# Optimization experiments

Measured on AMD Instinct MI355X. Metric: run time of the kernel, lower is better.

Reference implementation:

```python
import jax, jax.numpy as jnp
import numpy as np

B, D, H, S = 4096, 512, 512, 16
EVENT_THRESH = 0.85  # hard-coded in original forward (e_t > 0.85), tau unused


def setup_inputs() -> dict:
    key = jax.random.key(0)
    ks = jax.random.split(key, 17)
    s = 0.02
    return {
        "x_t": jax.random.normal(ks[0], (B, D), jnp.float32),
        "h_lstm": jax.random.normal(ks[1], (B, H), jnp.float32),
        "c_lstm": jax.random.normal(ks[2], (B, H), jnp.float32),
        "slots": jax.random.normal(ks[3], (B, S, D), jnp.float32),
        "ptr": jax.random.randint(ks[4], (B,), 0, S, jnp.int32),
        # SequenceMemoryCell params
        "value_W": jax.random.normal(ks[5], (D, D), jnp.float32) * s,
        "value_b": jnp.zeros((D,), jnp.float32),
        "ed_W": jax.random.normal(ks[6], (1, D), jnp.float32) * s,
        "ed_b": jnp.zeros((1,), jnp.float32),
        "pos_emb": jax.random.normal(ks[7], (S, D), jnp.float32),
        "lstm_Wih": jax.random.normal(ks[8], (4 * H, D), jnp.float32) * s,
        "lstm_Whh": jax.random.normal(ks[9], (4 * H, H), jnp.float32) * s,
        "lstm_bih": jnp.zeros((4 * H,), jnp.float32),
        "lstm_bhh": jnp.zeros((4 * H,), jnp.float32),
        # outer hand-written LSTM params
        "Wih": jax.random.normal(ks[10], (4 * H, D + H), jnp.float32) * s,
        "bih": jnp.zeros((4 * H,), jnp.float32),
        "Whh": jax.random.normal(ks[11], (4 * H, H), jnp.float32) * s,
    }


def reference(x_t, h_lstm, c_lstm, slots, value_W, value_b, ed_W, ed_b,
              pos_emb, lstm_Wih, lstm_Whh, lstm_bih, lstm_bhh,
              Wih, bih, Whh, ptr):
    b, n_slots, d = slots.shape
    h = lstm_Whh.shape[1]
    # --- SequenceMemoryCell ---
    e_t = jax.nn.sigmoid(x_t @ ed_W.T + ed_b)            # (B, 1)
    event = e_t > EVENT_THRESH                            # (B, 1) bool
    v = x_t @ value_W.T + value_b                         # (B, D)
    # conditional pointer-indexed write into circular slot buffer
    write = (jnp.arange(n_slots)[None, :] == ptr[:, None]) & event  # (B, S)
    new_slots = jnp.where(write[:, :, None], v[:, None, :], slots)
    new_ptr = (ptr + event[:, 0].astype(ptr.dtype)) % n_slots
    slots_pe = new_slots + pos_emb[None, :, :]            # (B, S, D)
    # slot-fuser LSTM over n_slots (PyTorch gate order i,f,g,o), h0=c0=0
    def step(carry, x_s):
        hh, cc = carry
        g = x_s @ lstm_Wih.T + lstm_bih + hh @ lstm_Whh.T + lstm_bhh
        i, f, gg, o = jnp.split(g, 4, axis=1)
        cc = jax.nn.sigmoid(f) * cc + jax.nn.sigmoid(i) * jnp.tanh(gg)
        hh = jax.nn.sigmoid(o) * jnp.tanh(cc)
        return (hh, cc), None
    h0 = jnp.zeros((b, h), slots.dtype)
    (h_mem, _), _ = jax.lax.scan(step, (h0, h0), jnp.swapaxes(slots_pe, 0, 1))
    # --- outer hand-written LSTM cell on [x_t; h_mem] ---
    gates = jnp.concatenate([x_t, h_mem], axis=1) @ Wih.T + bih + h_lstm @ Whh.T
    i, f, g_t, o = jnp.split(gates, 4, axis=1)
    c_new = jax.nn.sigmoid(f) * c_lstm + jax.nn.sigmoid(i) * jnp.tanh(g_t)
    h_new = jax.nn.sigmoid(o) * jnp.tanh(c_new)
    return (h_new, c_new, h_mem, new_slots, new_ptr)
```

## Files before the change

### kernel.cpp

```cpp
#include <hip/hip_runtime.h>
#include <hip/hip_bf16.h>

constexpr int kB = 4096;
constexpr int kD = 512;
constexpr int kH = 512;
constexpr int kS = 16;
constexpr int kG = 2048;

typedef __attribute__((ext_vector_type(8))) short bf16x8_t;
typedef __attribute__((ext_vector_type(4))) float f32x4_t;

__device__ __forceinline__ short f2bf(float x) {
  __hip_bfloat16 h = __float2bfloat16(x);
  return *reinterpret_cast<short*>(&h);
}
__device__ __forceinline__ float sigm(float x) { return 1.0f / (1.0f + expf(-x)); }

__global__ void event_kernel(const float* __restrict__ x,
                             const float* __restrict__ edW,
                             const float* __restrict__ edb,
                             const int* __restrict__ ptr,
                             int* __restrict__ ev,
                             float* __restrict__ newptr_out)
{
  int b = blockIdx.x * 4 + (threadIdx.x >> 6);
  int lane = threadIdx.x & 63;
  const float* xr = x + (size_t)b * kD;
  float sum = 0.f;
  for (int k = lane; k < kD; k += 64) sum += xr[k] * edW[k];
  #pragma unroll
  for (int off = 32; off; off >>= 1) sum += __shfl_down(sum, off, 64);
  if (lane == 0) {
    float e = sigm(sum + edb[0]);
    int evt = (e > 0.85f) ? 1 : 0;
    ev[b] = evt;
    newptr_out[b] = (float)((ptr[b] + evt) & (kS - 1));
  }
}

__global__ void f2b_kernel(const float* __restrict__ src, short* __restrict__ dst, int n4)
{
  int i = blockIdx.x * blockDim.x + threadIdx.x;
  if (i >= n4) return;
  const float4 v = reinterpret_cast<const float4*>(src)[i];
  short4 o;
  o.x = f2bf(v.x); o.y = f2bf(v.y); o.z = f2bf(v.z); o.w = f2bf(v.w);
  reinterpret_cast<short4*>(dst)[i] = o;
}

__global__ void packw_gates_kernel(const float* __restrict__ W1, int w1,
                                   const float* __restrict__ W2, int w2,
                                   short* __restrict__ dst, int total4)
{
  int i = blockIdx.x * blockDim.x + threadIdx.x;
  if (i >= total4) return;
  long e = (long)i * 4;
  int K = w1 + w2;
  long p = e / K;
  int col = (int)(e - p * K);
  long r = (long)(((p >> 4) & 3) * 512 + ((p >> 6) << 4) + (p & 15));
  const float* src = (col < w1) ? (W1 + r * (long)w1 + col)
                                : (W2 + r * (long)w2 + (col - w1));
  const float4 v = *reinterpret_cast<const float4*>(src);
  short4 o; o.x=f2bf(v.x); o.y=f2bf(v.y); o.z=f2bf(v.z); o.w=f2bf(v.w);
  *reinterpret_cast<short4*>(dst + e) = o;
}

__global__ void packbias_kernel(const float* __restrict__ b1, const float* __restrict__ b2,
                                float* __restrict__ o, int n)
{
  int p = blockIdx.x * blockDim.x + threadIdx.x;
  if (p >= n) return;
  int r = ((p >> 4) & 3) * 512 + ((p >> 6) << 4) + (p & 15);
  float v = b1[r];
  if (b2) v += b2[r];
  o[p] = v;
}

__global__ void slot_update_kernel(const float* __restrict__ slots,
                                   const float* __restrict__ v,
                                   const float* __restrict__ pos_emb,
                                   const int* __restrict__ ptr,
                                   const int* __restrict__ ev,
                                   float* __restrict__ new_slots,
                                   short* __restrict__ slots_pe)
{
  size_t i = (size_t)blockIdx.x * blockDim.x + threadIdx.x;
  size_t e = i * 4;
  int d = (int)(e & (kD - 1));
  size_t bs = e >> 9;
  int s = (int)(bs & (kS - 1));
  size_t b = bs >> 4;
  float4 val;
  if (ev[b] && (ptr[b] == s)) val = *reinterpret_cast<const float4*>(v + (b << 9) + d);
  else                        val = *reinterpret_cast<const float4*>(slots + e);
  *reinterpret_cast<float4*>(new_slots + e) = val;
  const float4 pe = *reinterpret_cast<const float4*>(pos_emb + ((size_t)s << 9) + d);
  short4 o;
  o.x = f2bf(val.x + pe.x); o.y = f2bf(val.y + pe.y);
  o.z = f2bf(val.z + pe.z); o.w = f2bf(val.w + pe.w);
  *reinterpret_cast<short4*>(slots_pe + e) = o;
}

__global__ __launch_bounds__(256)
void gemm_fused_kernel(const short* __restrict__ A0, int lda0,
                       const short* __restrict__ A1, int lda1,
                       const short* __restrict__ A2, int lda2,
                       int nseg, const short* __restrict__ W, int ldw,
                       const float* __restrict__ bias, int mode,
                       float* __restrict__ C, int ldc,
                       float* __restrict__ cbuf, short* __restrict__ hb,
                       float* __restrict__ hmem, int first, int last,
                       const float* __restrict__ c_in,
                       float* __restrict__ h_out, float* __restrict__ c_out)
{
  __shared__ short As[128 * 64];
  __shared__ short Ws[128 * 64];
  const int tid  = threadIdx.x;
  const int wave = tid >> 6;
  const int lane = tid & 63;
  const int wr = wave >> 1;
  const int wc = wave & 1;
  const int row0 = blockIdx.x * 128;
  const int col0 = blockIdx.y * 128;
  const int K = nseg << 9;

  f32x4_t acc[4][4];
  #pragma unroll
  for (int m = 0; m < 4; ++m)
    #pragma unroll
    for (int n = 0; n < 4; ++n)
      acc[m][n] = {0.f, 0.f, 0.f, 0.f};

  const int sr = lane >> 3;
  const int sc = (lane & 7) * 8;

  for (int k0 = 0; k0 < K; k0 += 64) {
    const int seg = k0 >> 9;
    const int ks  = k0 & 511;
    const short* Ap = (seg == 0) ? A0 : ((seg == 1) ? A1 : A2);
    const int   lda = (seg == 0) ? lda0 : ((seg == 1) ? lda1 : lda2);
    __syncthreads();
    #pragma unroll
    for (int j = 0; j < 4; ++j) {
      const int arow = wave * 32 + j * 8 + sr;
      const short* asrc = Ap + (size_t)(row0 + arow) * lda + ks + sc;
      __builtin_amdgcn_global_load_lds(
          (const __attribute__((address_space(1))) void*)asrc,
          (__attribute__((address_space(3))) void*)&As[(wave * 32 + j * 8) * 64],
          16, 0, 0);
      const short* wsrc = W + (size_t)(col0 + arow) * ldw + k0 + sc;
      __builtin_amdgcn_global_load_lds(
          (const __attribute__((address_space(1))) void*)wsrc,
          (__attribute__((address_space(3))) void*)&Ws[(wave * 32 + j * 8) * 64],
          16, 0, 0);
    }
    __syncthreads();
    #pragma unroll
    for (int kk = 0; kk < 64; kk += 32) {
      bf16x8_t af[4], bfr[4];
      const int kcol = kk + (lane >> 4) * 8;
      const int ar = wr * 64 + (lane & 15);
      const int br = wc * 64 + (lane & 15);
      #pragma unroll
      for (int m = 0; m < 4; ++m)
        af[m] = *reinterpret_cast<const bf16x8_t*>(&As[(ar + m * 16) * 64 + kcol]);
      #pragma unroll
      for (int n = 0; n < 4; ++n)
        bfr[n] = *reinterpret_cast<const bf16x8_t*>(&Ws[(br + n * 16) * 64 + kcol]);
      #pragma unroll
      for (int m = 0; m < 4; ++m)
        #pragma unroll
        for (int n = 0; n < 4; ++n)
          acc[m][n] = __builtin_amdgcn_mfma_f32_16x16x32_bf16(af[m], bfr[n], acc[m][n], 0, 0, 0);
    }
  }

  float bv[4];
  #pragma unroll
  for (int n = 0; n < 4; ++n)
    bv[n] = bias[col0 + wc * 64 + n * 16 + (lane & 15)];

  if (mode == 0) {
    #pragma unroll
    for (int n = 0; n < 4; ++n) {
      const int col = col0 + wc * 64 + n * 16 + (lane & 15);
      #pragma unroll
      for (int m = 0; m < 4; ++m) {
        const int rbase = row0 + wr * 64 + m * 16 + (lane >> 4) * 4;
        #pragma unroll
        for (int r = 0; r < 4; ++r)
          C[(size_t)(rbase + r) * ldc + col] = acc[m][n][r] + bv[n];
      }
    }
    return;
  }

  const int hcol = ((col0 >> 6) + wc) * 16 + (lane & 15);
  #pragma unroll
  for (int m = 0; m < 4; ++m) {
    const int rbase = row0 + wr * 64 + m * 16 + (lane >> 4) * 4;
    #pragma unroll
    for (int r = 0; r < 4; ++r) {
      const size_t idx = (size_t)(rbase + r) * kH + hcol;
      const float gi = acc[m][0][r] + bv[0];
      const float gf = acc[m][1][r] + bv[1];
      const float gg = acc[m][2][r] + bv[2];
      const float go = acc[m][3][r] + bv[3];
      float cp;
      if (mode == 1) cp = first ? 0.f : cbuf[idx];
      else           cp = c_in[idx];
      const float cn = sigm(gf) * cp + sigm(gi) * tanhf(gg);
      const float hn = sigm(go) * tanhf(cn);
      if (mode == 1) {
        cbuf[idx] = cn;
        hb[idx] = f2bf(hn);
        if (last) hmem[idx] = hn;
      } else {
        c_out[idx] = cn;
        h_out[idx] = hn;
      }
    }
  }
}

extern "C" void kernel_launch(void* const* d_in, const int* in_sizes, int n_in,
                              void* d_out, int out_size, void* d_ws, size_t ws_size,
                              hipStream_t stream)
{
  const float* x_t      = (const float*)d_in[0];
  const float* h_lstm   = (const float*)d_in[1];
  const float* c_lstm   = (const float*)d_in[2];
  const float* slots    = (const float*)d_in[3];
  const int*   ptr      = (const int*)  d_in[4];
  const float* value_W  = (const float*)d_in[5];
  const float* value_b  = (const float*)d_in[6];
  const float* ed_W     = (const float*)d_in[7];
  const float* ed_b     = (const float*)d_in[8];
  const float* pos_emb  = (const float*)d_in[9];
  const float* lstm_Wih = (const float*)d_in[10];
  const float* lstm_Whh = (const float*)d_in[11];
  const float* lstm_bih = (const float*)d_in[12];
  const float* lstm_bhh = (const float*)d_in[13];
  const float* Wih      = (const float*)d_in[14];
  const float* bih      = (const float*)d_in[15];
  const float* Whh      = (const float*)d_in[16];

  float* out       = (float*)d_out;
  float* h_new     = out;
  float* c_new     = out + (size_t)kB * kH;
  float* h_mem     = out + (size_t)2 * kB * kH;
  float* new_slots = out + (size_t)3 * kB * kH;
  float* new_ptr   = out + (size_t)3 * kB * kH + (size_t)kB * kS * kD;

  char* ws = (char*)d_ws;
  size_t off = 0;
  auto alloc = [&](size_t bytes) { void* p = ws + off; off += (bytes + 255) & ~(size_t)255; return p; };
  int*   ev        = (int*)  alloc((size_t)kB * 4);
  short* x_b       = (short*)alloc((size_t)kB * kD * 2);
  short* hlstm_b   = (short*)alloc((size_t)kB * kH * 2);
  short* vW_b      = (short*)alloc((size_t)kD * kD * 2);
  short* stepW_b   = (short*)alloc((size_t)kG * (kD + kH) * 2);
  float* stepBias  = (float*)alloc((size_t)kG * 4);
  short* outerW_b  = (short*)alloc((size_t)kG * (kD + kH + kH) * 2);
  float* outerBias = (float*)alloc((size_t)kG * 4);
  float* v_f32     = (float*)alloc((size_t)kB * kD * 4);
  short* h_b       = (short*)alloc((size_t)kB * kH * 2);
  float* c_f32     = (float*)alloc((size_t)kB * kH * 4);
  short* slots_pe  = (short*)alloc((size_t)kB * kS * kD * 2);
  (void)ws_size; (void)in_sizes; (void)n_in; (void)out_size;

  event_kernel<<<kB / 4, 256, 0, stream>>>(x_t, ed_W, ed_b, ptr, ev, new_ptr);

  f2b_kernel<<<(kB * kD / 4 + 255) / 256, 256, 0, stream>>>(x_t, x_b, kB * kD / 4);
  f2b_kernel<<<(kB * kH / 4 + 255) / 256, 256, 0, stream>>>(h_lstm, hlstm_b, kB * kH / 4);
  f2b_kernel<<<(kD * kD / 4 + 255) / 256, 256, 0, stream>>>(value_W, vW_b, kD * kD / 4);
  packw_gates_kernel<<<(kG * 1024 / 4 + 255) / 256, 256, 0, stream>>>(
      lstm_Wih, kD, lstm_Whh, kH, stepW_b, kG * 1024 / 4);
  packw_gates_kernel<<<(kG * 1536 / 4 + 255) / 256, 256, 0, stream>>>(
      Wih, kD + kH, Whh, kH, outerW_b, kG * 1536 / 4);
  packbias_kernel<<<(kG + 255) / 256, 256, 0, stream>>>(lstm_bih, lstm_bhh, stepBias, kG);
  packbias_kernel<<<(kG + 255) / 256, 256, 0, stream>>>(bih, nullptr, outerBias, kG);

  gemm_fused_kernel<<<dim3(kB / 128, kD / 128), 256, 0, stream>>>(
      x_b, kD, nullptr, 0, nullptr, 0, 1, vW_b, kD, value_b, 0,
      v_f32, kD, nullptr, nullptr, nullptr, 0, 0, nullptr, nullptr, nullptr);

  slot_update_kernel<<<(int)((size_t)kB * kS * kD / 4 / 256), 256, 0, stream>>>(
      slots, v_f32, pos_emb, ptr, ev, new_slots, slots_pe);

  for (int s = 0; s < kS; ++s) {
    const short* a0 = slots_pe + (size_t)s * kD;
    const int first = (s == 0) ? 1 : 0;
    const int last  = (s == kS - 1) ? 1 : 0;
    if (s == 0) {
      gemm_fused_kernel<<<dim3(kB / 128, kG / 128), 256, 0, stream>>>(
          a0, kS * kD, nullptr, 0, nullptr, 0, 1, stepW_b, kD + kH, stepBias, 1,
          nullptr, 0, c_f32, h_b, h_mem, first, last, nullptr, nullptr, nullptr);
    } else {
      gemm_fused_kernel<<<dim3(kB / 128, kG / 128), 256, 0, stream>>>(
          a0, kS * kD, h_b, kH, nullptr, 0, 2, stepW_b, kD + kH, stepBias, 1,
          nullptr, 0, c_f32, h_b, h_mem, first, last, nullptr, nullptr, nullptr);
    }
  }

  gemm_fused_kernel<<<dim3(kB / 128, kG / 128), 256, 0, stream>>>(
      x_b, kD, h_b, kH, hlstm_b, kH, 3, outerW_b, kD + kH + kH, outerBias, 2,
      nullptr, 0, nullptr, nullptr, nullptr, 0, 0, c_lstm, h_new, c_new);
}
```

Baseline: 748.7 us.

## Shrink GEMM tiles to 128x64 with XCD-aware block remapping

The fused GEMM tile drops from 128x128 to 128x64 outputs per block, so each wave now covers 32 rows by 64 columns, and the launch becomes a 1D grid. Block indices are remapped so that consecutive logical tiles land on the same XCD, for better L2 reuse of A and W. Launch bounds now request 4 blocks per CU. This doubles the block count to improve occupancy and latency hiding on the per-step LSTM GEMMs. The cost is lower data reuse per tile: more global and LDS traffic per FLOP.

```diff
diff --git a/kernel.cpp b/kernel.cpp
--- a/kernel.cpp
+++ b/kernel.cpp
@@ -102,12 +102,12 @@
   *reinterpret_cast<short4*>(slots_pe + e) = o;
 }
 
-__global__ __launch_bounds__(256)
+__global__ __launch_bounds__(256, 4)
 void gemm_fused_kernel(const short* __restrict__ A0, int lda0,
                        const short* __restrict__ A1, int lda1,
                        const short* __restrict__ A2, int lda2,
                        int nseg, const short* __restrict__ W, int ldw,
-                       const float* __restrict__ bias, int mode,
+                       const float* __restrict__ bias, int mode, int nby,
                        float* __restrict__ C, int ldc,
                        float* __restrict__ cbuf, short* __restrict__ hb,
                        float* __restrict__ hmem, int first, int last,
@@ -115,25 +115,28 @@
                        float* __restrict__ h_out, float* __restrict__ c_out)
 {
   __shared__ short As[128 * 64];
-  __shared__ short Ws[128 * 64];
+  __shared__ short Ws[64 * 64];
   const int tid  = threadIdx.x;
   const int wave = tid >> 6;
   const int lane = tid & 63;
-  const int wr = wave >> 1;
-  const int wc = wave & 1;
-  const int row0 = blockIdx.x * 128;
-  const int col0 = blockIdx.y * 128;
+
+  const int nb  = gridDim.x;
+  const int vid = (blockIdx.x & 7) * (nb >> 3) + (blockIdx.x >> 3);
+  const int bx  = vid / nby;
+  const int by  = vid - bx * nby;
+  const int row0 = bx * 128;
+  const int col0 = by * 64;
   const int K = nseg << 9;
 
-  f32x4_t acc[4][4];
+  f32x4_t acc[2][4];
   #pragma unroll
-  for (int m = 0; m < 4; ++m)
+  for (int m = 0; m < 2; ++m)
     #pragma unroll
     for (int n = 0; n < 4; ++n)
       acc[m][n] = {0.f, 0.f, 0.f, 0.f};
 
-  const int sr = lane >> 3;
-  const int sc = (lane & 7) * 8;
+  const int srow = tid >> 3;
+  const int scol = (tid & 7) * 8;
 
   for (int k0 = 0; k0 < K; k0 += 64) {
     const int seg = k0 >> 9;
@@ -143,33 +146,37 @@
     __syncthreads();
     #pragma unroll
     for (int j = 0; j < 4; ++j) {
-      const int arow = wave * 32 + j * 8 + sr;
-      const short* asrc = Ap + (size_t)(row0 + arow) * lda + ks + sc;
+      const int arow = j * 32 + srow;
+      const short* asrc = Ap + (size_t)(row0 + arow) * lda + ks + scol;
       __builtin_amdgcn_global_load_lds(
           (const __attribute__((address_space(1))) void*)asrc,
-          (__attribute__((address_space(3))) void*)&As[(wave * 32 + j * 8) * 64],
+          (__attribute__((address_space(3))) void*)&As[arow * 64 + scol],
           16, 0, 0);
-      const short* wsrc = W + (size_t)(col0 + arow) * ldw + k0 + sc;
+    }
+    #pragma unroll
+    for (int j = 0; j < 2; ++j) {
+      const int wrow = j * 32 + srow;
+      const short* wsrc = W + (size_t)(col0 + wrow) * ldw + k0 + scol;
       __builtin_amdgcn_global_load_lds(
           (const __attribute__((address_space(1))) void*)wsrc,
-          (__attribute__((address_space(3))) void*)&Ws[(wave * 32 + j * 8) * 64],
+          (__attribute__((address_space(3))) void*)&Ws[wrow * 64 + scol],
           16, 0, 0);
     }
     __syncthreads();
     #pragma unroll
     for (int kk = 0; kk < 64; kk += 32) {
-      bf16x8_t af[4], bfr[4];
+      bf16x8_t af[2], bfr[4];
       const int kcol = kk + (lane >> 4) * 8;
-      const int ar = wr * 64 + (lane & 15);
-      const int br = wc * 64 + (lane & 15);
+      const int ar = wave * 32 + (lane & 15);
+      const int br = lane & 15;
       #pragma unroll
-      for (int m = 0; m < 4; ++m)
+      for (int m = 0; m < 2; ++m)
         af[m] = *reinterpret_cast<const bf16x8_t*>(&As[(ar + m * 16) * 64 + kcol]);
       #pragma unroll
       for (int n = 0; n < 4; ++n)
         bfr[n] = *reinterpret_cast<const bf16x8_t*>(&Ws[(br + n * 16) * 64 + kcol]);
       #pragma unroll
-      for (int m = 0; m < 4; ++m)
+      for (int m = 0; m < 2; ++m)
         #pragma unroll
         for (int n = 0; n < 4; ++n)
           acc[m][n] = __builtin_amdgcn_mfma_f32_16x16x32_bf16(af[m], bfr[n], acc[m][n], 0, 0, 0);
@@ -179,15 +186,15 @@
   float bv[4];
   #pragma unroll
   for (int n = 0; n < 4; ++n)
-    bv[n] = bias[col0 + wc * 64 + n * 16 + (lane & 15)];
+    bv[n] = bias[col0 + n * 16 + (lane & 15)];
 
   if (mode == 0) {
     #pragma unroll
     for (int n = 0; n < 4; ++n) {
-      const int col = col0 + wc * 64 + n * 16 + (lane & 15);
+      const int col = col0 + n * 16 + (lane & 15);
       #pragma unroll
-      for (int m = 0; m < 4; ++m) {
-        const int rbase = row0 + wr * 64 + m * 16 + (lane >> 4) * 4;
+      for (int m = 0; m < 2; ++m) {
+        const int rbase = row0 + wave * 32 + m * 16 + (lane >> 4) * 4;
         #pragma unroll
         for (int r = 0; r < 4; ++r)
           C[(size_t)(rbase + r) * ldc + col] = acc[m][n][r] + bv[n];
@@ -196,10 +203,10 @@
     return;
   }
 
-  const int hcol = ((col0 >> 6) + wc) * 16 + (lane & 15);
+  const int hcol = (col0 >> 6) * 16 + (lane & 15);
   #pragma unroll
-  for (int m = 0; m < 4; ++m) {
-    const int rbase = row0 + wr * 64 + m * 16 + (lane >> 4) * 4;
+  for (int m = 0; m < 2; ++m) {
+    const int rbase = row0 + wave * 32 + m * 16 + (lane >> 4) * 4;
     #pragma unroll
     for (int r = 0; r < 4; ++r) {
       const size_t idx = (size_t)(rbase + r) * kH + hcol;
@@ -282,8 +289,8 @@
   packbias_kernel<<<(kG + 255) / 256, 256, 0, stream>>>(lstm_bih, lstm_bhh, stepBias, kG);
   packbias_kernel<<<(kG + 255) / 256, 256, 0, stream>>>(bih, nullptr, outerBias, kG);
 
-  gemm_fused_kernel<<<dim3(kB / 128, kD / 128), 256, 0, stream>>>(
-      x_b, kD, nullptr, 0, nullptr, 0, 1, vW_b, kD, value_b, 0,
+  gemm_fused_kernel<<<(kB / 128) * (kD / 64), 256, 0, stream>>>(
+      x_b, kD, nullptr, 0, nullptr, 0, 1, vW_b, kD, value_b, 0, kD / 64,
       v_f32, kD, nullptr, nullptr, nullptr, 0, 0, nullptr, nullptr, nullptr);
 
   slot_update_kernel<<<(int)((size_t)kB * kS * kD / 4 / 256), 256, 0, stream>>>(
@@ -294,17 +301,17 @@
     const int first = (s == 0) ? 1 : 0;
     const int last  = (s == kS - 1) ? 1 : 0;
     if (s == 0) {
-      gemm_fused_kernel<<<dim3(kB / 128, kG / 128), 256, 0, stream>>>(
-          a0, kS * kD, nullptr, 0, nullptr, 0, 1, stepW_b, kD + kH, stepBias, 1,
+      gemm_fused_kernel<<<(kB / 128) * (kG / 64), 256, 0, stream>>>(
+          a0, kS * kD, nullptr, 0, nullptr, 0, 1, stepW_b, kD + kH, stepBias, 1, kG / 64,
           nullptr, 0, c_f32, h_b, h_mem, first, last, nullptr, nullptr, nullptr);
     } else {
-      gemm_fused_kernel<<<dim3(kB / 128, kG / 128), 256, 0, stream>>>(
-          a0, kS * kD, h_b, kH, nullptr, 0, 2, stepW_b, kD + kH, stepBias, 1,
+      gemm_fused_kernel<<<(kB / 128) * (kG / 64), 256, 0, stream>>>(
+          a0, kS * kD, h_b, kH, nullptr, 0, 2, stepW_b, kD + kH, stepBias, 1, kG / 64,
           nullptr, 0, c_f32, h_b, h_mem, first, last, nullptr, nullptr, nullptr);
     }
   }
 
-  gemm_fused_kernel<<<dim3(kB / 128, kG / 128), 256, 0, stream>>>(
-      x_b, kD, h_b, kH, hlstm_b, kH, 3, outerW_b, kD + kH + kH, outerBias, 2,
+  gemm_fused_kernel<<<(kB / 128) * (kG / 64), 256, 0, stream>>>(
+      x_b, kD, h_b, kH, hlstm_b, kH, 3, outerW_b, kD + kH + kH, outerBias, 2, kG / 64,
       nullptr, 0, nullptr, nullptr, nullptr, 0, 0, c_lstm, h_new, c_new);
 }
```

New measurement: 688.8 us. -8.0%, faster.
